# Kernel tuning notes

Hardware: AMD Instinct MI355X
Metric: run time of the kernel (lower is better)

Reference implementation:

```python
import jax, jax.numpy as jnp
import numpy as np

N_NODES = 50000
N_EDGES = 800000
D_IN = 128
D_HID = 128
N_CLS = 47


def setup_inputs() -> dict:
    key = jax.random.key(0)
    ks = jax.random.split(key, 10)
    inp = {
        "features": jax.random.normal(ks[0], (N_NODES, D_IN), dtype=jnp.float32),
        "src": jax.random.randint(ks[1], (N_EDGES,), 0, N_NODES),
        "dst": jax.random.randint(ks[2], (N_EDGES,), 0, N_NODES),
        "Wself0": jax.random.normal(ks[3], (D_IN, D_HID), dtype=jnp.float32) / np.sqrt(D_IN),
        "Wneigh0": jax.random.normal(ks[4], (D_IN, D_HID), dtype=jnp.float32) / np.sqrt(D_IN),
        "b0": jnp.zeros((D_HID,), dtype=jnp.float32),
        "Wself1": jax.random.normal(ks[5], (D_HID, D_HID), dtype=jnp.float32) / np.sqrt(D_HID),
        "Wneigh1": jax.random.normal(ks[6], (D_HID, D_HID), dtype=jnp.float32) / np.sqrt(D_HID),
        "b1": jnp.zeros((D_HID,), dtype=jnp.float32),
        "Wself2": jax.random.normal(ks[7], (D_HID, N_CLS), dtype=jnp.float32) / np.sqrt(D_HID),
        "Wneigh2": jax.random.normal(ks[8], (D_HID, N_CLS), dtype=jnp.float32) / np.sqrt(D_HID),
        "b2": jnp.zeros((N_CLS,), dtype=jnp.float32),
    }
    return inp


def reference(features, src, dst, Wself0, Wneigh0, b0, Wself1, Wneigh1, b1, Wself2, Wneigh2, b2):
    # GraphSAGE (DGL SAGEConv, aggregator_type='mean', eval mode so dropout is identity).
    # Per layer: h_neigh[v] = mean_{(u->v) in E} h[u]; out = h @ W_self + h_neigh @ W_neigh + b
    n = features.shape[0]
    # in-degree for mean aggregation (zero-degree nodes get zero neighbor feature)
    deg = jax.ops.segment_sum(jnp.ones(dst.shape, dtype=features.dtype), dst, num_segments=n)
    inv_deg = (1.0 / jnp.maximum(deg, 1.0))[:, None]  # [N,1]

    def sage_layer(h, Ws, Wn, b, act):
        # gather src features per edge, scatter-add into dst, normalize by in-degree
        agg = jax.ops.segment_sum(h[src], dst, num_segments=n) * inv_deg  # [N, d]
        out = h @ Ws + agg @ Wn + b
        return jax.nn.relu(out) if act else out

    h = sage_layer(features, Wself0, Wneigh0, b0, True)
    h = sage_layer(h, Wself1, Wneigh1, b1, True)
    h = sage_layer(h, Wself2, Wneigh2, b2, False)
    return h
```

## Files before the change

### kernel.cpp

```cpp
#include <hip/hip_runtime.h>

#define D 128
#define NCLS 47

typedef short short8 __attribute__((ext_vector_type(8)));
typedef float floatx4 __attribute__((ext_vector_type(4)));

__device__ __forceinline__ float bf16lo(unsigned int u) {
    union { unsigned int i; float f; } c; c.i = u << 16; return c.f;
}
__device__ __forceinline__ float bf16hi(unsigned int u) {
    union { unsigned int i; float f; } c; c.i = u & 0xffff0000u; return c.f;
}
__device__ __forceinline__ unsigned short f2bf(float f) {
    union { float f; unsigned int i; } c; c.f = f;
    unsigned int r = c.i + 0x7fffu + ((c.i >> 16) & 1u);
    return (unsigned short)(r >> 16);
}
__device__ __forceinline__ unsigned int pack2(float x, float y) {
    return (unsigned int)f2bf(x) | ((unsigned int)f2bf(y) << 16);
}

__device__ __forceinline__ void acc8(uint4 u, float* a) {
    a[0] += bf16lo(u.x); a[1] += bf16hi(u.x);
    a[2] += bf16lo(u.y); a[3] += bf16hi(u.y);
    a[4] += bf16lo(u.z); a[5] += bf16hi(u.z);
    a[6] += bf16lo(u.w); a[7] += bf16hi(u.w);
}

#define FBm 1024
__global__ __launch_bounds__(256) void fill_prep_kernel(
    const int* __restrict__ src, const int* __restrict__ dst,
    int* __restrict__ cnt0, int* __restrict__ cnt1,
    unsigned short* __restrict__ csr, int n_edges,
    const float* __restrict__ f, unsigned int* __restrict__ hA, int npairs, int n,
    const float* __restrict__ Ws0, const float* __restrict__ Wn0, unsigned short* __restrict__ Wt0,
    const float* __restrict__ Ws1, const float* __restrict__ Wn1, unsigned short* __restrict__ Wt1,
    const float* __restrict__ Ws2, const float* __restrict__ Wn2, unsigned short* __restrict__ Wt2) {
    if (blockIdx.x < FBm) {
        int cohort = blockIdx.x & 7;
        int cb = blockIdx.x >> 3;
        int nth = (FBm >> 3) * 256;
        int tid = cb * 256 + threadIdx.x;
        int range = (n + 7) >> 3;
        int lo = cohort * range;
        int hi = lo + range;
        if (hi > n) hi = n;
        const int4* dst4 = (const int4*)dst;
        int nq = n_edges >> 2;
        for (int q = tid; q < nq; q += nth) {
            int4 dd = dst4[q];
            int e = q << 2;
            if (dd.x >= lo && dd.x < hi) {
                int p = atomicAdd(&cnt0[dd.x], 1);
                if (p < 32) csr[dd.x * 64 + p] = (unsigned short)src[e];
            }
            if (dd.y >= lo && dd.y < hi) {
                int p = atomicAdd(&cnt1[dd.y], 1);
                if (p < 32) csr[dd.y * 64 + 32 + p] = (unsigned short)src[e + 1];
            }
            if (dd.z >= lo && dd.z < hi) {
                int p = atomicAdd(&cnt0[dd.z], 1);
                if (p < 32) csr[dd.z * 64 + p] = (unsigned short)src[e + 2];
            }
            if (dd.w >= lo && dd.w < hi) {
                int p = atomicAdd(&cnt1[dd.w], 1);
                if (p < 32) csr[dd.w * 64 + 32 + p] = (unsigned short)src[e + 3];
            }
        }
        for (int e = (nq << 2) + tid; e < n_edges; e += nth) {
            int d = dst[e];
            if (d >= lo && d < hi) {
                if (e & 1) {
                    int p = atomicAdd(&cnt1[d], 1);
                    if (p < 32) csr[d * 64 + 32 + p] = (unsigned short)src[e];
                } else {
                    int p = atomicAdd(&cnt0[d], 1);
                    if (p < 32) csr[d * 64 + p] = (unsigned short)src[e];
                }
            }
        }
        return;
    }
    int tid = (blockIdx.x - FBm) * 256 + threadIdx.x;
    int stride = (gridDim.x - FBm) * 256;
    int total = npairs + 2 * 128 * 256 + 48 * 256;
    for (int gid = tid; gid < total; gid += stride) {
        if (gid < npairs) {
            float2 v = ((const float2*)f)[gid];
            hA[gid] = pack2(v.x, v.y);
            continue;
        }
        int r = gid - npairs;
        if (r < 128 * 256) {
            int nn = r >> 8, k = r & 255;
            float v = (k < 128) ? Ws0[k * 128 + nn] : Wn0[(k - 128) * 128 + nn];
            Wt0[nn * 256 + k] = f2bf(v);
            continue;
        }
        r -= 128 * 256;
        if (r < 128 * 256) {
            int nn = r >> 8, k = r & 255;
            float v = (k < 128) ? Ws1[k * 128 + nn] : Wn1[(k - 128) * 128 + nn];
            Wt1[nn * 256 + k] = f2bf(v);
            continue;
        }
        r -= 128 * 256;
        if (r < 48 * 256) {
            int nn = r >> 8, k = r & 255;
            float v = 0.0f;
            if (nn < NCLS) v = (k < 128) ? Ws2[k * NCLS + nn] : Wn2[(k - 128) * NCLS + nn];
            Wt2[nn * 256 + k] = f2bf(v);
        }
    }
}

__global__ __launch_bounds__(256) void sage_fused_kernel(
    const unsigned int* __restrict__ hin,
    const unsigned short* __restrict__ csr,
    const int* __restrict__ cnt0,
    const int* __restrict__ cnt1,
    const unsigned short* __restrict__ Wt,
    const float* __restrict__ bias,
    unsigned short* __restrict__ hout,
    float* __restrict__ out,
    int n, int mode) {
    __shared__ unsigned int selfl[16][68];
    __shared__ unsigned int aggl[16][68];
    __shared__ __align__(16) unsigned short idxl[16][64];
    __shared__ int dl[16];

    int wave = threadIdx.x >> 6;
    int lane = threadIdx.x & 63;
    int base = blockIdx.x * 16;
    const uint4* hin4 = (const uint4*)hin;

    {
        int rowi = threadIdx.x >> 4;
        int q = threadIdx.x & 15;
        int ns = base + rowi;
        uint4 sv; sv.x = 0u; sv.y = 0u; sv.z = 0u; sv.w = 0u;
        int c0 = 0, c1 = 0;
        if (ns < n) {
            sv = hin4[(size_t)ns * 16 + q];
            c0 = cnt0[ns]; if (c0 > 32) c0 = 32;
            c1 = cnt1[ns]; if (c1 > 32) c1 = 32;
        }
        *(uint4*)&selfl[rowi][q * 4] = sv;
        int d = c0 + c1;
        const unsigned short* crow = csr + (size_t)ns * 64;
        unsigned int w0 = 0, w1 = 0;
        int j = q * 4;
        if (j < d)     w0  = (unsigned int)crow[j     < c0 ? j     : 32 + j     - c0];
        if (j + 1 < d) w0 |= (unsigned int)crow[j + 1 < c0 ? j + 1 : 32 + j + 1 - c0] << 16;
        if (j + 2 < d) w1  = (unsigned int)crow[j + 2 < c0 ? j + 2 : 32 + j + 2 - c0];
        if (j + 3 < d) w1 |= (unsigned int)crow[j + 3 < c0 ? j + 3 : 32 + j + 3 - c0] << 16;
        unsigned int* ip = (unsigned int*)&idxl[rowi][0];
        ip[q * 2] = w0;
        ip[q * 2 + 1] = w1;
        if (q == 0) dl[rowi] = d;
    }
    __syncthreads();

    int g = lane >> 4;
    int fl = lane & 15;
    int li = wave * 4 + g;
    int d = dl[li];
    const unsigned short* myidx = &idxl[li][0];

    float a[8];
#pragma unroll
    for (int j = 0; j < 8; ++j) a[j] = 0.0f;

    int k = 0;
    for (; k + 8 <= d; k += 8) {
        uint4 iq = *(const uint4*)(myidx + k);
        unsigned i0 = iq.x & 0xffffu, i1 = iq.x >> 16;
        unsigned i2 = iq.y & 0xffffu, i3 = iq.y >> 16;
        unsigned i4 = iq.z & 0xffffu, i5 = iq.z >> 16;
        unsigned i6 = iq.w & 0xffffu, i7 = iq.w >> 16;
        uint4 u0 = hin4[(size_t)i0 * 16 + fl];
        uint4 u1 = hin4[(size_t)i1 * 16 + fl];
        uint4 u2 = hin4[(size_t)i2 * 16 + fl];
        uint4 u3 = hin4[(size_t)i3 * 16 + fl];
        uint4 u4 = hin4[(size_t)i4 * 16 + fl];
        uint4 u5 = hin4[(size_t)i5 * 16 + fl];
        uint4 u6 = hin4[(size_t)i6 * 16 + fl];
        uint4 u7 = hin4[(size_t)i7 * 16 + fl];
        acc8(u0, a); acc8(u1, a); acc8(u2, a); acc8(u3, a);
        acc8(u4, a); acc8(u5, a); acc8(u6, a); acc8(u7, a);
    }
    if (k + 4 <= d) {
        uint2 iq = *(const uint2*)(myidx + k);
        unsigned i0 = iq.x & 0xffffu, i1 = iq.x >> 16;
        unsigned i2 = iq.y & 0xffffu, i3 = iq.y >> 16;
        uint4 u0 = hin4[(size_t)i0 * 16 + fl];
        uint4 u1 = hin4[(size_t)i1 * 16 + fl];
        uint4 u2 = hin4[(size_t)i2 * 16 + fl];
        uint4 u3 = hin4[(size_t)i3 * 16 + fl];
        acc8(u0, a); acc8(u1, a); acc8(u2, a); acc8(u3, a);
        k += 4;
    }
    for (; k < d; ++k) {
        unsigned idx = myidx[k];
        uint4 u = hin4[(size_t)idx * 16 + fl];
        acc8(u, a);
    }

    {
        float inv = 1.0f / fmaxf((float)d, 1.0f);
        uint4 o;
        o.x = pack2(a[0] * inv, a[1] * inv);
        o.y = pack2(a[2] * inv, a[3] * inv);
        o.z = pack2(a[4] * inv, a[5] * inv);
        o.w = pack2(a[6] * inv, a[7] * inv);
        *(uint4*)&aggl[li][fl * 4] = o;
    }
    __syncthreads();

    int m = lane & 15;
    int quad = lane >> 4;
    int t0 = (mode == 2) ? wave : wave * 2;
    int ntt = (mode == 2) ? ((wave < 3) ? 1 : 0) : 2;
    const unsigned short* arow = (const unsigned short*)&selfl[m][0];
    const unsigned short* lrow = (const unsigned short*)&aggl[m][0];

    floatx4 acc[2];
    acc[0] = (floatx4){0.f, 0.f, 0.f, 0.f};
    acc[1] = (floatx4){0.f, 0.f, 0.f, 0.f};

    if (ntt > 0) {
#pragma unroll
        for (int ko = 0; ko < 128; ko += 32) {
            short8 a = *(const short8*)(arow + ko + quad * 8);
            for (int tt = 0; tt < ntt; ++tt) {
                short8 bfr = *(const short8*)(Wt + (size_t)((t0 + tt) * 16 + m) * 256 + ko + quad * 8);
                acc[tt] = __builtin_amdgcn_mfma_f32_16x16x32_bf16(a, bfr, acc[tt], 0, 0, 0);
            }
        }
#pragma unroll
        for (int ko = 0; ko < 128; ko += 32) {
            short8 a = *(const short8*)(lrow + ko + quad * 8);
            for (int tt = 0; tt < ntt; ++tt) {
                short8 bfr = *(const short8*)(Wt + (size_t)((t0 + tt) * 16 + m) * 256 + 128 + ko + quad * 8);
                acc[tt] = __builtin_amdgcn_mfma_f32_16x16x32_bf16(a, bfr, acc[tt], 0, 0, 0);
            }
        }

        if (mode == 1) {
            for (int tt = 0; tt < ntt; ++tt) {
                int nfeat = (t0 + tt) * 16 + m;
                float bb = bias[nfeat];
#pragma unroll
                for (int r = 0; r < 4; ++r) {
                    int node = base + quad * 4 + r;
                    if (node < n) {
                        float v = fmaxf(acc[tt][r] + bb, 0.0f);
                        hout[(size_t)node * 128 + nfeat] = f2bf(v);
                    }
                }
            }
        } else {
            int nfeat = t0 * 16 + m;
            if (nfeat < NCLS) {
                float bb = bias[nfeat];
#pragma unroll
                for (int r = 0; r < 4; ++r) {
                    int node = base + quad * 4 + r;
                    if (node < n) out[(size_t)node * NCLS + nfeat] = acc[0][r] + bb;
                }
            }
        }
    }
}

extern "C" void kernel_launch(void* const* d_in, const int* in_sizes, int n_in,
                              void* d_out, int out_size, void* d_ws, size_t ws_size,
                              hipStream_t stream) {
    const float* features = (const float*)d_in[0];
    const int* src = (const int*)d_in[1];
    const int* dst = (const int*)d_in[2];
    const float* Ws0 = (const float*)d_in[3];
    const float* Wn0 = (const float*)d_in[4];
    const float* b0 = (const float*)d_in[5];
    const float* Ws1 = (const float*)d_in[6];
    const float* Wn1 = (const float*)d_in[7];
    const float* b1 = (const float*)d_in[8];
    const float* Ws2 = (const float*)d_in[9];
    const float* Wn2 = (const float*)d_in[10];
    const float* b2 = (const float*)d_in[11];
    float* out = (float*)d_out;

    int n = in_sizes[0] / D;
    int n_edges = in_sizes[1];

    int* cnt0 = (int*)d_ws;
    int* cnt1 = cnt0 + 50048;
    unsigned short* csr = (unsigned short*)(cnt1 + 50048);
    unsigned int* hA = (unsigned int*)(csr + (size_t)n * 64 + 32);
    unsigned int* hB = hA + (size_t)n * 64;
    unsigned short* Wt0 = (unsigned short*)(hB + (size_t)n * 64);
    unsigned short* Wt1 = Wt0 + 128 * 256;
    unsigned short* Wt2 = Wt1 + 128 * 256;

    int npairs = n * 64;

    hipMemsetAsync(cnt0, 0, (size_t)2 * 50048 * sizeof(int), stream);
    fill_prep_kernel<<<2048, 256, 0, stream>>>(
        src, dst, cnt0, cnt1, csr, n_edges, features, hA, npairs, n,
        Ws0, Wn0, Wt0, Ws1, Wn1, Wt1, Ws2, Wn2, Wt2);

    int tiles = (n + 15) / 16;

    sage_fused_kernel<<<tiles, 256, 0, stream>>>(hA, csr, cnt0, cnt1, Wt0, b0,
                                                 (unsigned short*)hB, nullptr, n, 1);
    sage_fused_kernel<<<tiles, 256, 0, stream>>>(hB, csr, cnt0, cnt1, Wt1, b1,
                                                 (unsigned short*)hA, nullptr, n, 1);
    sage_fused_kernel<<<tiles, 256, 0, stream>>>(hA, csr, cnt0, cnt1, Wt2, b2,
                                                 nullptr, out, n, 2);
}
```

Baseline: 295.2 us.

## Project last layer before aggregation, use sentinel zero row, process 32-node tiles

For the final layer, neighbor features are first projected through W_neigh (128→64 padded) by a new proj_kernel, so aggregation gathers 64-wide bf16 rows instead of 128-wide. A zero sentinel row at index n replaces the tail loops, letting each 16-lane group gather two nodes' neighbor lists in lockstep up to the max degree. Tiles grow to 32 nodes per block with a launch_bounds occupancy hint. The trade-off is an extra kernel launch and wasted gathers of the sentinel row when the two nodes' degrees differ.

```diff
diff --git a/kernel.cpp b/kernel.cpp
--- a/kernel.cpp
+++ b/kernel.cpp
@@ -27,13 +27,18 @@
     a[4] += bf16lo(u.z); a[5] += bf16hi(u.z);
     a[6] += bf16lo(u.w); a[7] += bf16hi(u.w);
 }
+__device__ __forceinline__ void acc4(uint2 u, float* a) {
+    a[0] += bf16lo(u.x); a[1] += bf16hi(u.x);
+    a[2] += bf16lo(u.y); a[3] += bf16hi(u.y);
+}
 
 #define FBm 1024
 __global__ __launch_bounds__(256) void fill_prep_kernel(
     const int* __restrict__ src, const int* __restrict__ dst,
     int* __restrict__ cnt0, int* __restrict__ cnt1,
     unsigned short* __restrict__ csr, int n_edges,
-    const float* __restrict__ f, unsigned int* __restrict__ hA, int npairs, int n,
+    const float* __restrict__ f, unsigned int* __restrict__ hA,
+    unsigned int* __restrict__ hBz, int npairs, int n,
     const float* __restrict__ Ws0, const float* __restrict__ Wn0, unsigned short* __restrict__ Wt0,
     const float* __restrict__ Ws1, const float* __restrict__ Wn1, unsigned short* __restrict__ Wt1,
     const float* __restrict__ Ws2, const float* __restrict__ Wn2, unsigned short* __restrict__ Wt2) {
@@ -84,11 +89,15 @@
     }
     int tid = (blockIdx.x - FBm) * 256 + threadIdx.x;
     int stride = (gridDim.x - FBm) * 256;
-    int total = npairs + 2 * 128 * 256 + 48 * 256;
+    int total = npairs + 2 * 128 * 256 + 64 * 256 + 64;
     for (int gid = tid; gid < total; gid += stride) {
         if (gid < npairs) {
-            float2 v = ((const float2*)f)[gid];
-            hA[gid] = pack2(v.x, v.y);
+            if (gid < npairs - 64) {
+                float2 v = ((const float2*)f)[gid];
+                hA[gid] = pack2(v.x, v.y);
+            } else {
+                hA[gid] = 0u;
+            }
             continue;
         }
         int r = gid - npairs;
@@ -106,17 +115,21 @@
             continue;
         }
         r -= 128 * 256;
-        if (r < 48 * 256) {
+        if (r < 64 * 256) {
             int nn = r >> 8, k = r & 255;
             float v = 0.0f;
             if (nn < NCLS) v = (k < 128) ? Ws2[k * NCLS + nn] : Wn2[(k - 128) * NCLS + nn];
             Wt2[nn * 256 + k] = f2bf(v);
-        }
-    }
-}
-
-__global__ __launch_bounds__(256) void sage_fused_kernel(
-    const unsigned int* __restrict__ hin,
+            continue;
+        }
+        r -= 64 * 256;
+        if (r < 64) hBz[(size_t)n * 64 + r] = 0u;
+    }
+}
+
+__global__ __launch_bounds__(256, 4) void sage_fused_kernel(
+    const unsigned int* __restrict__ hself,
+    const unsigned int* __restrict__ hagg,
     const unsigned short* __restrict__ csr,
     const int* __restrict__ cnt0,
     const int* __restrict__ cnt1,
@@ -125,152 +138,233 @@
     unsigned short* __restrict__ hout,
     float* __restrict__ out,
     int n, int mode) {
-    __shared__ unsigned int selfl[16][68];
-    __shared__ unsigned int aggl[16][68];
-    __shared__ __align__(16) unsigned short idxl[16][64];
-    __shared__ int dl[16];
+    __shared__ unsigned int selfl[32][68];
+    __shared__ unsigned int aggl[32][68];
+    __shared__ __align__(16) unsigned short idxl[32][64];
+    __shared__ int dl[32];
 
     int wave = threadIdx.x >> 6;
     int lane = threadIdx.x & 63;
-    int base = blockIdx.x * 16;
-    const uint4* hin4 = (const uint4*)hin;
-
+    int base = blockIdx.x * 32;
+    const uint4* hs4 = (const uint4*)hself;
+
+    {
+        int rowi0 = threadIdx.x >> 4;
+        int q = threadIdx.x & 15;
+        unsigned sent = (unsigned)n;
+#pragma unroll
+        for (int j2 = 0; j2 < 2; ++j2) {
+            int rowi = rowi0 + j2 * 16;
+            int ns = base + rowi;
+            uint4 sv; sv.x = 0u; sv.y = 0u; sv.z = 0u; sv.w = 0u;
+            int c0 = 0, c1 = 0;
+            if (ns < n) {
+                sv = hs4[(size_t)ns * 16 + q];
+                c0 = cnt0[ns]; if (c0 > 32) c0 = 32;
+                c1 = cnt1[ns]; if (c1 > 32) c1 = 32;
+            }
+            *(uint4*)&selfl[rowi][q * 4] = sv;
+            int d = c0 + c1;
+            const unsigned short* crow = csr + (size_t)ns * 64;
+            int j = q * 4;
+            unsigned e0 = (j     < d) ? (unsigned)crow[j     < c0 ? j     : 32 + j     - c0] : sent;
+            unsigned e1 = (j + 1 < d) ? (unsigned)crow[j + 1 < c0 ? j + 1 : 32 + j + 1 - c0] : sent;
+            unsigned e2 = (j + 2 < d) ? (unsigned)crow[j + 2 < c0 ? j + 2 : 32 + j + 2 - c0] : sent;
+            unsigned e3 = (j + 3 < d) ? (unsigned)crow[j + 3 < c0 ? j + 3 : 32 + j + 3 - c0] : sent;
+            unsigned int* ip = (unsigned int*)&idxl[rowi][0];
+            ip[q * 2]     = e0 | (e1 << 16);
+            ip[q * 2 + 1] = e2 | (e3 << 16);
+            if (q == 0) dl[rowi] = d;
+        }
+    }
+    __syncthreads();
+
+    int sg = lane >> 4;
+    int fl = lane & 15;
+    int liA = (wave * 4 + sg) * 2;
+    int liB = liA + 1;
+    int dA = dl[liA], dB = dl[liB];
+    const unsigned short* iA = &idxl[liA][0];
+    const unsigned short* iB = &idxl[liB][0];
+    int cm = dA > dB ? dA : dB;
+    float invA = 1.0f / fmaxf((float)dA, 1.0f);
+    float invB = 1.0f / fmaxf((float)dB, 1.0f);
+
+    if (mode == 1) {
+        const uint4* hg4 = (const uint4*)hagg;
+        float a[8], b[8];
+#pragma unroll
+        for (int j = 0; j < 8; ++j) { a[j] = 0.f; b[j] = 0.f; }
+        for (int k = 0; k < cm; k += 8) {
+            uint4 qa = *(const uint4*)(iA + k);
+            uint4 qb = *(const uint4*)(iB + k);
+            unsigned a0 = qa.x & 0xffffu, a1 = qa.x >> 16, a2 = qa.y & 0xffffu, a3 = qa.y >> 16;
+            unsigned a4 = qa.z & 0xffffu, a5 = qa.z >> 16, a6 = qa.w & 0xffffu, a7 = qa.w >> 16;
+            unsigned b0 = qb.x & 0xffffu, b1 = qb.x >> 16, b2 = qb.y & 0xffffu, b3 = qb.y >> 16;
+            unsigned b4 = qb.z & 0xffffu, b5 = qb.z >> 16, b6 = qb.w & 0xffffu, b7 = qb.w >> 16;
+            uint4 uA0 = hg4[(size_t)a0 * 16 + fl], uA1 = hg4[(size_t)a1 * 16 + fl];
+            uint4 uA2 = hg4[(size_t)a2 * 16 + fl], uA3 = hg4[(size_t)a3 * 16 + fl];
+            uint4 uA4 = hg4[(size_t)a4 * 16 + fl], uA5 = hg4[(size_t)a5 * 16 + fl];
+            uint4 uA6 = hg4[(size_t)a6 * 16 + fl], uA7 = hg4[(size_t)a7 * 16 + fl];
+            uint4 uB0 = hg4[(size_t)b0 * 16 + fl], uB1 = hg4[(size_t)b1 * 16 + fl];
+            uint4 uB2 = hg4[(size_t)b2 * 16 + fl], uB3 = hg4[(size_t)b3 * 16 + fl];
+            uint4 uB4 = hg4[(size_t)b4 * 16 + fl], uB5 = hg4[(size_t)b5 * 16 + fl];
+            uint4 uB6 = hg4[(size_t)b6 * 16 + fl], uB7 = hg4[(size_t)b7 * 16 + fl];
+            acc8(uA0, a); acc8(uA1, a); acc8(uA2, a); acc8(uA3, a);
+            acc8(uA4, a); acc8(uA5, a); acc8(uA6, a); acc8(uA7, a);
+            acc8(uB0, b); acc8(uB1, b); acc8(uB2, b); acc8(uB3, b);
+            acc8(uB4, b); acc8(uB5, b); acc8(uB6, b); acc8(uB7, b);
+        }
+        uint4 oA, oB;
+        oA.x = pack2(a[0] * invA, a[1] * invA); oA.y = pack2(a[2] * invA, a[3] * invA);
+        oA.z = pack2(a[4] * invA, a[5] * invA); oA.w = pack2(a[6] * invA, a[7] * invA);
+        oB.x = pack2(b[0] * invB, b[1] * invB); oB.y = pack2(b[2] * invB, b[3] * invB);
+        oB.z = pack2(b[4] * invB, b[5] * invB); oB.w = pack2(b[6] * invB, b[7] * invB);
+        *(uint4*)&aggl[liA][fl * 4] = oA;
+        *(uint4*)&aggl[liB][fl * 4] = oB;
+    } else {
+        const uint2* hg2 = (const uint2*)hagg;
+        float a[4], b[4];
+#pragma unroll
+        for (int j = 0; j < 4; ++j) { a[j] = 0.f; b[j] = 0.f; }
+        for (int k = 0; k < cm; k += 8) {
+            uint4 qa = *(const uint4*)(iA + k);
+            uint4 qb = *(const uint4*)(iB + k);
+            unsigned a0 = qa.x & 0xffffu, a1 = qa.x >> 16, a2 = qa.y & 0xffffu, a3 = qa.y >> 16;
+            unsigned a4 = qa.z & 0xffffu, a5 = qa.z >> 16, a6 = qa.w & 0xffffu, a7 = qa.w >> 16;
+            unsigned b0 = qb.x & 0xffffu, b1 = qb.x >> 16, b2 = qb.y & 0xffffu, b3 = qb.y >> 16;
+            unsigned b4 = qb.z & 0xffffu, b5 = qb.z >> 16, b6 = qb.w & 0xffffu, b7 = qb.w >> 16;
+            uint2 uA0 = hg2[(size_t)a0 * 16 + fl], uA1 = hg2[(size_t)a1 * 16 + fl];
+            uint2 uA2 = hg2[(size_t)a2 * 16 + fl], uA3 = hg2[(size_t)a3 * 16 + fl];
+            uint2 uA4 = hg2[(size_t)a4 * 16 + fl], uA5 = hg2[(size_t)a5 * 16 + fl];
+            uint2 uA6 = hg2[(size_t)a6 * 16 + fl], uA7 = hg2[(size_t)a7 * 16 + fl];
+            uint2 uB0 = hg2[(size_t)b0 * 16 + fl], uB1 = hg2[(size_t)b1 * 16 + fl];
+            uint2 uB2 = hg2[(size_t)b2 * 16 + fl], uB3 = hg2[(size_t)b3 * 16 + fl];
+            uint2 uB4 = hg2[(size_t)b4 * 16 + fl], uB5 = hg2[(size_t)b5 * 16 + fl];
+            uint2 uB6 = hg2[(size_t)b6 * 16 + fl], uB7 = hg2[(size_t)b7 * 16 + fl];
+            acc4(uA0, a); acc4(uA1, a); acc4(uA2, a); acc4(uA3, a);
+            acc4(uA4, a); acc4(uA5, a); acc4(uA6, a); acc4(uA7, a);
+            acc4(uB0, b); acc4(uB1, b); acc4(uB2, b); acc4(uB3, b);
+            acc4(uB4, b); acc4(uB5, b); acc4(uB6, b); acc4(uB7, b);
+        }
+        float* fA = (float*)&aggl[liA][0];
+        float* fB = (float*)&aggl[liB][0];
+        fA[fl * 4 + 0] = a[0] * invA; fA[fl * 4 + 1] = a[1] * invA;
+        fA[fl * 4 + 2] = a[2] * invA; fA[fl * 4 + 3] = a[3] * invA;
+        fB[fl * 4 + 0] = b[0] * invB; fB[fl * 4 + 1] = b[1] * invB;
+        fB[fl * 4 + 2] = b[2] * invB; fB[fl * 4 + 3] = b[3] * invB;
+    }
+    __syncthreads();
+
+    int m = lane & 15;
+    int quad = lane >> 4;
+    int mt = wave & 1;
+    int strip = wave >> 1;
+    const unsigned short* arow = (const unsigned short*)&selfl[mt * 16 + m][0];
+
+    if (mode == 1) {
+        const unsigned short* lrow = (const unsigned short*)&aggl[mt * 16 + m][0];
+        int t0 = strip * 4;
+        floatx4 acc[4];
+#pragma unroll
+        for (int tt = 0; tt < 4; ++tt) acc[tt] = (floatx4){0.f, 0.f, 0.f, 0.f};
+#pragma unroll
+        for (int ko = 0; ko < 128; ko += 32) {
+            short8 av = *(const short8*)(arow + ko + quad * 8);
+#pragma unroll
+            for (int tt = 0; tt < 4; ++tt) {
+                short8 bfr = *(const short8*)(Wt + (size_t)((t0 + tt) * 16 + m) * 256 + ko + quad * 8);
+                acc[tt] = __builtin_amdgcn_mfma_f32_16x16x32_bf16(av, bfr, acc[tt], 0, 0, 0);
+            }
+        }
+#pragma unroll
+        for (int ko = 0; ko < 128; ko += 32) {
+            short8 av = *(const short8*)(lrow + ko + quad * 8);
+#pragma unroll
+            for (int tt = 0; tt < 4; ++tt) {
+                short8 bfr = *(const short8*)(Wt + (size_t)((t0 + tt) * 16 + m) * 256 + 128 + ko + quad * 8);
+                acc[tt] = __builtin_amdgcn_mfma_f32_16x16x32_bf16(av, bfr, acc[tt], 0, 0, 0);
+            }
+        }
+#pragma unroll
+        for (int tt = 0; tt < 4; ++tt) {
+            int nfeat = (t0 + tt) * 16 + m;
+            float bb = bias[nfeat];
+#pragma unroll
+            for (int r = 0; r < 4; ++r) {
+                int node = base + mt * 16 + quad * 4 + r;
+                if (node < n) {
+                    float v = fmaxf(acc[tt][r] + bb, 0.0f);
+                    hout[(size_t)node * 128 + nfeat] = f2bf(v);
+                }
+            }
+        }
+    } else {
+        int t0 = strip * 2;
+        floatx4 acc[2];
+        acc[0] = (floatx4){0.f, 0.f, 0.f, 0.f};
+        acc[1] = (floatx4){0.f, 0.f, 0.f, 0.f};
+#pragma unroll
+        for (int ko = 0; ko < 128; ko += 32) {
+            short8 av = *(const short8*)(arow + ko + quad * 8);
+#pragma unroll
+            for (int tt = 0; tt < 2; ++tt) {
+                short8 bfr = *(const short8*)(Wt + (size_t)((t0 + tt) * 16 + m) * 256 + ko + quad * 8);
+                acc[tt] = __builtin_amdgcn_mfma_f32_16x16x32_bf16(av, bfr, acc[tt], 0, 0, 0);
+            }
+        }
+#pragma unroll
+        for (int tt = 0; tt < 2; ++tt) {
+            int nfeat = (t0 + tt) * 16 + m;
+            if (nfeat < NCLS) {
+                float bb = bias[nfeat];
+#pragma unroll
+                for (int r = 0; r < 4; ++r) {
+                    int node = base + mt * 16 + quad * 4 + r;
+                    if (node < n) {
+                        const float* fr = (const float*)&aggl[mt * 16 + quad * 4 + r][0];
+                        out[(size_t)node * NCLS + nfeat] = acc[tt][r] + fr[nfeat] + bb;
+                    }
+                }
+            }
+        }
+    }
+}
+
+__global__ __launch_bounds__(256) void proj_kernel(
+    const unsigned int* __restrict__ hin,
+    const unsigned short* __restrict__ Wt,
+    unsigned short* __restrict__ P,
+    int np) {
+    __shared__ unsigned int sl[16][68];
+    int wave = threadIdx.x >> 6;
+    int lane = threadIdx.x & 63;
+    int pb = blockIdx.x * 16;
+    const uint4* h4 = (const uint4*)hin;
     {
         int rowi = threadIdx.x >> 4;
         int q = threadIdx.x & 15;
-        int ns = base + rowi;
+        int ns = pb + rowi;
         uint4 sv; sv.x = 0u; sv.y = 0u; sv.z = 0u; sv.w = 0u;
-        int c0 = 0, c1 = 0;
-        if (ns < n) {
-            sv = hin4[(size_t)ns * 16 + q];
-            c0 = cnt0[ns]; if (c0 > 32) c0 = 32;
-            c1 = cnt1[ns]; if (c1 > 32) c1 = 32;
-        }
-        *(uint4*)&selfl[rowi][q * 4] = sv;
-        int d = c0 + c1;
-        const unsigned short* crow = csr + (size_t)ns * 64;
-        unsigned int w0 = 0, w1 = 0;
-        int j = q * 4;
-        if (j < d)     w0  = (unsigned int)crow[j     < c0 ? j     : 32 + j     - c0];
-        if (j + 1 < d) w0 |= (unsigned int)crow[j + 1 < c0 ? j + 1 : 32 + j + 1 - c0] << 16;
-        if (j + 2 < d) w1  = (unsigned int)crow[j + 2 < c0 ? j + 2 : 32 + j + 2 - c0];
-        if (j + 3 < d) w1 |= (unsigned int)crow[j + 3 < c0 ? j + 3 : 32 + j + 3 - c0] << 16;
-        unsigned int* ip = (unsigned int*)&idxl[rowi][0];
-        ip[q * 2] = w0;
-        ip[q * 2 + 1] = w1;
-        if (q == 0) dl[rowi] = d;
+        if (ns < np) sv = h4[(size_t)ns * 16 + q];
+        *(uint4*)&sl[rowi][q * 4] = sv;
     }
     __syncthreads();
-
-    int g = lane >> 4;
-    int fl = lane & 15;
-    int li = wave * 4 + g;
-    int d = dl[li];
-    const unsigned short* myidx = &idxl[li][0];
-
-    float a[8];
-#pragma unroll
-    for (int j = 0; j < 8; ++j) a[j] = 0.0f;
-
-    int k = 0;
-    for (; k + 8 <= d; k += 8) {
-        uint4 iq = *(const uint4*)(myidx + k);
-        unsigned i0 = iq.x & 0xffffu, i1 = iq.x >> 16;
-        unsigned i2 = iq.y & 0xffffu, i3 = iq.y >> 16;
-        unsigned i4 = iq.z & 0xffffu, i5 = iq.z >> 16;
-        unsigned i6 = iq.w & 0xffffu, i7 = iq.w >> 16;
-        uint4 u0 = hin4[(size_t)i0 * 16 + fl];
-        uint4 u1 = hin4[(size_t)i1 * 16 + fl];
-        uint4 u2 = hin4[(size_t)i2 * 16 + fl];
-        uint4 u3 = hin4[(size_t)i3 * 16 + fl];
-        uint4 u4 = hin4[(size_t)i4 * 16 + fl];
-        uint4 u5 = hin4[(size_t)i5 * 16 + fl];
-        uint4 u6 = hin4[(size_t)i6 * 16 + fl];
-        uint4 u7 = hin4[(size_t)i7 * 16 + fl];
-        acc8(u0, a); acc8(u1, a); acc8(u2, a); acc8(u3, a);
-        acc8(u4, a); acc8(u5, a); acc8(u6, a); acc8(u7, a);
-    }
-    if (k + 4 <= d) {
-        uint2 iq = *(const uint2*)(myidx + k);
-        unsigned i0 = iq.x & 0xffffu, i1 = iq.x >> 16;
-        unsigned i2 = iq.y & 0xffffu, i3 = iq.y >> 16;
-        uint4 u0 = hin4[(size_t)i0 * 16 + fl];
-        uint4 u1 = hin4[(size_t)i1 * 16 + fl];
-        uint4 u2 = hin4[(size_t)i2 * 16 + fl];
-        uint4 u3 = hin4[(size_t)i3 * 16 + fl];
-        acc8(u0, a); acc8(u1, a); acc8(u2, a); acc8(u3, a);
-        k += 4;
-    }
-    for (; k < d; ++k) {
-        unsigned idx = myidx[k];
-        uint4 u = hin4[(size_t)idx * 16 + fl];
-        acc8(u, a);
-    }
-
-    {
-        float inv = 1.0f / fmaxf((float)d, 1.0f);
-        uint4 o;
-        o.x = pack2(a[0] * inv, a[1] * inv);
-        o.y = pack2(a[2] * inv, a[3] * inv);
-        o.z = pack2(a[4] * inv, a[5] * inv);
-        o.w = pack2(a[6] * inv, a[7] * inv);
-        *(uint4*)&aggl[li][fl * 4] = o;
-    }
-    __syncthreads();
-
     int m = lane & 15;
     int quad = lane >> 4;
-    int t0 = (mode == 2) ? wave : wave * 2;
-    int ntt = (mode == 2) ? ((wave < 3) ? 1 : 0) : 2;
-    const unsigned short* arow = (const unsigned short*)&selfl[m][0];
-    const unsigned short* lrow = (const unsigned short*)&aggl[m][0];
-
-    floatx4 acc[2];
-    acc[0] = (floatx4){0.f, 0.f, 0.f, 0.f};
-    acc[1] = (floatx4){0.f, 0.f, 0.f, 0.f};
-
-    if (ntt > 0) {
-#pragma unroll
-        for (int ko = 0; ko < 128; ko += 32) {
-            short8 a = *(const short8*)(arow + ko + quad * 8);
-            for (int tt = 0; tt < ntt; ++tt) {
-                short8 bfr = *(const short8*)(Wt + (size_t)((t0 + tt) * 16 + m) * 256 + ko + quad * 8);
-                acc[tt] = __builtin_amdgcn_mfma_f32_16x16x32_bf16(a, bfr, acc[tt], 0, 0, 0);
-            }
-        }
-#pragma unroll
-        for (int ko = 0; ko < 128; ko += 32) {
-            short8 a = *(const short8*)(lrow + ko + quad * 8);
-            for (int tt = 0; tt < ntt; ++tt) {
-                short8 bfr = *(const short8*)(Wt + (size_t)((t0 + tt) * 16 + m) * 256 + 128 + ko + quad * 8);
-                acc[tt] = __builtin_amdgcn_mfma_f32_16x16x32_bf16(a, bfr, acc[tt], 0, 0, 0);
-            }
-        }
-
-        if (mode == 1) {
-            for (int tt = 0; tt < ntt; ++tt) {
-                int nfeat = (t0 + tt) * 16 + m;
-                float bb = bias[nfeat];
-#pragma unroll
-                for (int r = 0; r < 4; ++r) {
-                    int node = base + quad * 4 + r;
-                    if (node < n) {
-                        float v = fmaxf(acc[tt][r] + bb, 0.0f);
-                        hout[(size_t)node * 128 + nfeat] = f2bf(v);
-                    }
-                }
-            }
-        } else {
-            int nfeat = t0 * 16 + m;
-            if (nfeat < NCLS) {
-                float bb = bias[nfeat];
-#pragma unroll
-                for (int r = 0; r < 4; ++r) {
-                    int node = base + quad * 4 + r;
-                    if (node < n) out[(size_t)node * NCLS + nfeat] = acc[0][r] + bb;
-                }
-            }
-        }
+    const unsigned short* arow = (const unsigned short*)&sl[m][0];
+    floatx4 acc = (floatx4){0.f, 0.f, 0.f, 0.f};
+#pragma unroll
+    for (int ko = 0; ko < 128; ko += 32) {
+        short8 av = *(const short8*)(arow + ko + quad * 8);
+        short8 bfr = *(const short8*)(Wt + (size_t)(wave * 16 + m) * 256 + 128 + ko + quad * 8);
+        acc = __builtin_amdgcn_mfma_f32_16x16x32_bf16(av, bfr, acc, 0, 0, 0);
+    }
+    int col = wave * 16 + m;
+#pragma unroll
+    for (int r = 0; r < 4; ++r) {
+        int node = pb + quad * 4 + r;
+        if (node < np) P[(size_t)node * 64 + col] = f2bf(acc[r]);
     }
 }
 
@@ -293,29 +387,32 @@
 
     int n = in_sizes[0] / D;
     int n_edges = in_sizes[1];
+    int np1 = n + 1;
 
     int* cnt0 = (int*)d_ws;
     int* cnt1 = cnt0 + 50048;
     unsigned short* csr = (unsigned short*)(cnt1 + 50048);
     unsigned int* hA = (unsigned int*)(csr + (size_t)n * 64 + 32);
-    unsigned int* hB = hA + (size_t)n * 64;
-    unsigned short* Wt0 = (unsigned short*)(hB + (size_t)n * 64);
+    unsigned int* hB = hA + (size_t)np1 * 64;
+    unsigned short* Wt0 = (unsigned short*)(hB + (size_t)np1 * 64);
     unsigned short* Wt1 = Wt0 + 128 * 256;
     unsigned short* Wt2 = Wt1 + 128 * 256;
-
-    int npairs = n * 64;
+    unsigned short* P = (unsigned short*)hB;
+
+    int npairs = np1 * 64;
 
     hipMemsetAsync(cnt0, 0, (size_t)2 * 50048 * sizeof(int), stream);
     fill_prep_kernel<<<2048, 256, 0, stream>>>(
-        src, dst, cnt0, cnt1, csr, n_edges, features, hA, npairs, n,
+        src, dst, cnt0, cnt1, csr, n_edges, features, hA, hB, npairs, n,
         Ws0, Wn0, Wt0, Ws1, Wn1, Wt1, Ws2, Wn2, Wt2);
 
-    int tiles = (n + 15) / 16;
-
-    sage_fused_kernel<<<tiles, 256, 0, stream>>>(hA, csr, cnt0, cnt1, Wt0, b0,
+    int tiles = (n + 31) / 32;
+
+    sage_fused_kernel<<<tiles, 256, 0, stream>>>(hA, hA, csr, cnt0, cnt1, Wt0, b0,
                                                  (unsigned short*)hB, nullptr, n, 1);
-    sage_fused_kernel<<<tiles, 256, 0, stream>>>(hB, csr, cnt0, cnt1, Wt1, b1,
+    sage_fused_kernel<<<tiles, 256, 0, stream>>>(hB, hB, csr, cnt0, cnt1, Wt1, b1,
                                                  (unsigned short*)hA, nullptr, n, 1);
-    sage_fused_kernel<<<tiles, 256, 0, stream>>>(hA, csr, cnt0, cnt1, Wt2, b2,
-                                                 nullptr, out, n, 2);
-}
+    proj_kernel<<<(np1 + 15) / 16, 256, 0, stream>>>(hA, Wt2, P, np1);
+    sage_fused_kernel<<<tiles, 256, 0, stream>>>(hA, (const unsigned int*)P, csr, cnt0, cnt1,
+                                                 Wt2, b2, nullptr, out, n, 2);
+}
```

Measured after the change: 289.9 us. No clear change (-1.8%).
